# Kernel optimization log

Measured on AMD Instinct MI355X. Metric: run time of the kernel, lower is better.

The kernel has to match this reference:

```python
import jax, jax.numpy as jnp
import numpy as np

N_LEADS = 12
N_HEADS = 4
LN_EPS = 1e-5

def _ecg_adj_norm():
    # Fixed 12-lead ECG adjacency with self loops, symmetric GCN normalization
    conns = [(0,1),(0,2),(1,2),(0,3),(1,3),(2,3),(0,4),(1,4),(1,5),(2,5),
             (6,7),(7,8),(8,9),(9,10),(10,11),(0,6),(1,9),(2,11)]
    A = np.zeros((N_LEADS, N_LEADS), dtype=np.float32)
    for i, j in conns:
        A[i, j] = 1.0
        A[j, i] = 1.0
    A += np.eye(N_LEADS, dtype=np.float32)
    d = A.sum(axis=1)
    dinv = 1.0 / np.sqrt(d)
    return jnp.asarray(dinv[:, None] * A * dinv[None, :])  # [12,12]

A_NORM = _ecg_adj_norm()

def gcn(x, W, b):
    # x: [B,12,F] -> A_norm @ (x W) + b
    return jnp.einsum('ij,bjf->bif', A_NORM, x @ W) + b

def mha(x, in_w, in_b, out_w, out_b):
    # x: [B,S,E]; torch nn.MultiheadAttention, batch_first=True
    B, S, E = x.shape
    D = E // N_HEADS
    qkv = x @ in_w.T + in_b                      # [B,S,3E]
    q, k, v = jnp.split(qkv, 3, axis=-1)
    def heads(t):
        return t.reshape(B, S, N_HEADS, D).transpose(0, 2, 1, 3)  # [B,H,S,D]
    q, k, v = heads(q), heads(k), heads(v)
    scores = jnp.einsum('bhsd,bhtd->bhst', q, k) / jnp.sqrt(jnp.float32(D))
    attn = jax.nn.softmax(scores, axis=-1)
    o = jnp.einsum('bhst,bhtd->bhsd', attn, v)   # [B,H,S,D]
    o = o.transpose(0, 2, 1, 3).reshape(B, S, E)
    return o @ out_w.T + out_b

def layer_norm(x, g, b):
    mu = x.mean(axis=-1, keepdims=True)
    var = ((x - mu) ** 2).mean(axis=-1, keepdims=True)
    return (x - mu) * jax.lax.rsqrt(var + LN_EPS) * g + b

def setup_inputs() -> dict:
    key = jax.random.key(0)
    ks = jax.random.split(key, 8)
    B, F_IN, H, OUT = 8192, 512, 256, 256
    s = lambda fan: 1.0 / np.sqrt(fan)
    return {
        'x': jax.random.normal(ks[0], (B, N_LEADS, F_IN), dtype=jnp.float32),
        'W1': jax.random.normal(ks[1], (F_IN, H), dtype=jnp.float32) * s(F_IN),
        'b1': jnp.zeros((H,), jnp.float32),
        'W2': jax.random.normal(ks[2], (H, H), dtype=jnp.float32) * s(H),
        'b2': jnp.zeros((H,), jnp.float32),
        'W3': jax.random.normal(ks[3], (H, OUT), dtype=jnp.float32) * s(H),
        'b3': jnp.zeros((OUT,), jnp.float32),
        'in_proj_w': jax.random.normal(ks[4], (3 * H, H), dtype=jnp.float32) * s(H),
        'in_proj_b': jnp.zeros((3 * H,), jnp.float32),
        'out_proj_w': jax.random.normal(ks[5], (H, H), dtype=jnp.float32) * s(H),
        'out_proj_b': jnp.zeros((H,), jnp.float32),
        'ln_g': jnp.ones((H,), jnp.float32),
        'ln_b': jnp.zeros((H,), jnp.float32),
    }

def reference(x, W1, b1, W2, b2, W3, b3, in_proj_w, in_proj_b, out_proj_w, out_proj_b, ln_g, ln_b):
    h = jax.nn.relu(gcn(x, W1, b1))              # dropout is identity at eval
    h = jax.nn.relu(gcn(h, W2, b2))              # [B,12,H]
    att = mha(h, in_proj_w, in_proj_b, out_proj_w, out_proj_b)
    h = layer_norm(h + att, ln_g, ln_b)
    h3 = gcn(h, W3, b3)                          # [B,12,OUT]
    w = jax.nn.softmax(h3.mean(axis=-1), axis=1) # [B,12] attention pooling
    x_weighted = jnp.einsum('bno,bn->bo', h3, w)
    x_max = h3.max(axis=1)
    return jnp.concatenate([x_weighted, x_max], axis=1)  # [B, 2*OUT]
```

## Files before the change

### kernel.cpp

```cpp
#include <hip/hip_runtime.h>
#include <hip/hip_bf16.h>
#include <cstdint>
#include <cstddef>

typedef unsigned short u16;
typedef u16 u16x8 __attribute__((ext_vector_type(8)));
typedef u16 u16x4 __attribute__((ext_vector_type(4)));
typedef __bf16 bf16x8 __attribute__((ext_vector_type(8)));
typedef float f32x4 __attribute__((ext_vector_type(4)));

__device__ const unsigned short ADJ_MASK[12] = {
    95u, 575u, 2095u, 15u, 19u, 38u, 193u, 448u, 896u, 1794u, 3584u, 3076u};

__device__ __forceinline__ float b2f(u16 u) {
  union { unsigned int i; float f; } v;
  v.i = ((unsigned int)u) << 16;
  return v.f;
}
__device__ __forceinline__ u16 f2b(float f) {
  union { float f; unsigned int i; } v;
  v.f = f;
  unsigned int r = v.i + 0x7fffu + ((v.i >> 16) & 1u);
  return (u16)(r >> 16);
}

#define GLOAD_LDS16(gsrc, ldst)                                         \
  __builtin_amdgcn_global_load_lds(                                     \
      (const __attribute__((address_space(1))) unsigned int*)(gsrc),    \
      (__attribute__((address_space(3))) unsigned int*)(ldst), 16, 0, 0)

__device__ __forceinline__ void build_anorm(float* An) {
  int t = threadIdx.x;
  if (t < 144) {
    int i = t / 12, j = t % 12;
    float di = (float)__popc((int)ADJ_MASK[i]);
    float dj = (float)__popc((int)ADJ_MASK[j]);
    An[t] = ((ADJ_MASK[i] >> j) & 1) ? (1.0f / sqrtf(di * dj)) : 0.0f;
  }
}

__global__ void __launch_bounds__(256) k_detect2(const void* a, const void* b,
                                                 int* flags) {
  const unsigned int* w = (const unsigned int*)(blockIdx.x ? b : a);
  __shared__ int s;
  if (threadIdx.x == 0) s = 0;
  __syncthreads();
  int cnt = 0;
  for (int t = 0; t < 16; ++t) {
    unsigned int v = w[t * 256 + threadIdx.x];
    unsigned int e = (v >> 7) & 0xFFu;
    if (e != 0u && (e < 0x5Au || e > 0x89u)) ++cnt;
  }
  atomicAdd(&s, cnt);
  __syncthreads();
  if (threadIdx.x == 0) flags[blockIdx.x] = (s > 1024) ? 1 : 0;
}

__global__ void __launch_bounds__(256) k_cvt_small(
    const void* b1, const void* b2, const void* b3, const void* inb,
    const void* outb, const void* lng, const void* lnb, u16* dst,
    const int* flag) {
  int idx = blockIdx.x * 256 + threadIdx.x;
  if (idx >= 2304) return;
  const void* src;
  int off = idx;
  if (idx < 256)       { src = b1; }
  else if (idx < 512)  { src = b2;   off = idx - 256; }
  else if (idx < 768)  { src = b3;   off = idx - 512; }
  else if (idx < 1536) { src = inb;  off = idx - 768; }
  else if (idx < 1792) { src = outb; off = idx - 1536; }
  else if (idx < 2048) { src = lng;  off = idx - 1792; }
  else                 { src = lnb;  off = idx - 2048; }
  dst[idx] = (*flag) ? f2b(((const float*)src)[off]) : ((const u16*)src)[off];
}

__global__ void __launch_bounds__(256) k_cvt_w(const void* inw,
                                               const void* outw, u16* dst,
                                               const int* flag) {
  int idx = blockIdx.x * 256 + threadIdx.x;
  const void* src = (idx < 196608) ? inw : outw;
  int off = (idx < 196608) ? idx : idx - 196608;
  dst[idx] = (*flag) ? f2b(((const float*)src)[off]) : ((const u16*)src)[off];
}

__global__ void __launch_bounds__(256) k_transpose3(const void* W1,
                                                    const void* W2,
                                                    const void* W3, u16* dst,
                                                    const int* flag) {
  int idx = blockIdx.x * 256 + threadIdx.x;
  const void* src;
  int R, C, li = idx;
  if (idx < 131072)      { src = W1; R = 512; C = 256; }
  else if (idx < 196608) { src = W2; R = 256; C = 256; li = idx - 131072; }
  else                   { src = W3; R = 256; C = 256; li = idx - 196608; }
  int c = li / R, r = li - c * R;
  u16 v = (*flag) ? f2b(((const float*)src)[r * C + c])
                  : ((const u16*)src)[r * C + c];
  dst[(idx - li) + c * R + r] = v;
}

__global__ void __launch_bounds__(256) k_mix(const u16* __restrict__ in,
                                             const u16* __restrict__ bias,
                                             u16* __restrict__ out, int relu) {
  __shared__ u16 X[6144];
  __shared__ float An[144];
  build_anorm(An);
  const int tid = threadIdx.x;
  const long base = (long)blockIdx.x * 6144;
#pragma unroll
  for (int i = 0; i < 3; ++i) {
    int idx = i * 256 + tid;
    *(u16x8*)(X + idx * 8) = *(const u16x8*)(in + base + idx * 8);
  }
  __syncthreads();
#pragma unroll
  for (int v = 0; v < 3; ++v) {
    int idx = v * 256 + tid;
    int s = idx / 384;
    int rem = idx - s * 384;
    int i = rem >> 5;
    int fg = rem & 31;
    float a[8];
#pragma unroll
    for (int u = 0; u < 8; ++u) a[u] = b2f(bias[fg * 8 + u]);
    for (int j = 0; j < 12; ++j) {
      float c = An[i * 12 + j];
      if (c != 0.0f) {
        u16x8 y = *(const u16x8*)(X + (s * 12 + j) * 256 + fg * 8);
#pragma unroll
        for (int u = 0; u < 8; ++u) a[u] += c * b2f(y[u]);
      }
    }
    u16x8 o;
#pragma unroll
    for (int u = 0; u < 8; ++u) {
      float vv = relu ? fmaxf(a[u], 0.0f) : a[u];
      o[u] = f2b(vv);
    }
    *(u16x8*)(out + base + idx * 8) = o;
  }
}

__device__ __forceinline__ void gemm_core(const void* __restrict__ A, int lda,
                                          int isf32,
                                          const u16* __restrict__ Bt,
                                          u16* As, u16* Bs,
                                          long m0, long n0, int K,
                                          f32x4 acc[6][4]) {
  const int tid = threadIdx.x;
  const int wave = tid >> 6, lane = tid & 63;
  const int q = lane >> 4, r16 = lane & 15;
  f32x4 zero = {0.f, 0.f, 0.f, 0.f};
#pragma unroll
  for (int a = 0; a < 6; ++a)
#pragma unroll
    for (int b = 0; b < 4; ++b) acc[a][b] = zero;

  for (int k0 = 0; k0 < K; k0 += 64) {
    if (isf32) {
      const float* Af = (const float*)A;
#pragma unroll
      for (int i = 0; i < 3; ++i) {
        int idx = i * 256 + tid;
        int rr = idx >> 3, cg = idx & 7;
        const float* sp = Af + (m0 + rr) * (long)lda + k0 + cg * 8;
        u16x8 t;
#pragma unroll
        for (int u = 0; u < 8; ++u) t[u] = f2b(sp[u]);
        *(u16x8*)(As + rr * 64 + ((cg ^ (rr & 7)) << 3)) = t;
      }
    } else {
      const u16* Ab = (const u16*)A;
#pragma unroll
      for (int i = 0; i < 3; ++i) {
        int c = i * 256 + tid;
        int rr = c >> 3, s = c & 7;
        GLOAD_LDS16(Ab + (m0 + rr) * (long)lda + k0 + ((s ^ (rr & 7)) << 3),
                    As + c * 8);
      }
    }
#pragma unroll
    for (int i = 0; i < 8; ++i) {
      int c = i * 256 + tid;
      int rr = c >> 3, s = c & 7;
      GLOAD_LDS16(Bt + (n0 + rr) * (long)K + k0 + ((s ^ (rr & 7)) << 3),
                  Bs + c * 8);
    }
    __syncthreads();
#pragma unroll
    for (int ks = 0; ks < 64; ks += 32) {
      const int ck = q + (ks >> 3);
      bf16x8 af[6], bfv[4];
#pragma unroll
      for (int rb = 0; rb < 6; ++rb) {
        int row = rb * 16 + r16;
        af[rb] = *(const bf16x8*)(As + row * 64 + ((ck ^ (row & 7)) << 3));
      }
#pragma unroll
      for (int cb = 0; cb < 4; ++cb) {
        int row = (wave * 4 + cb) * 16 + r16;
        bfv[cb] = *(const bf16x8*)(Bs + row * 64 + ((ck ^ (row & 7)) << 3));
      }
#pragma unroll
      for (int rb = 0; rb < 6; ++rb)
#pragma unroll
        for (int cb = 0; cb < 4; ++cb)
          acc[rb][cb] = __builtin_amdgcn_mfma_f32_16x16x32_bf16(
              af[rb], bfv[cb], acc[rb][cb], 0, 0, 0);
    }
    __syncthreads();
  }
}

__device__ __forceinline__ void gemm_core128(const void* __restrict__ A,
                                             int lda, int isf32,
                                             const u16* __restrict__ Bt,
                                             u16* As, u16* Bs,
                                             long m0, long n0, int K,
                                             f32x4 acc[6][2]) {
  const int tid = threadIdx.x;
  const int wave = tid >> 6, lane = tid & 63;
  const int q = lane >> 4, r16 = lane & 15;
  f32x4 zero = {0.f, 0.f, 0.f, 0.f};
#pragma unroll
  for (int a = 0; a < 6; ++a)
#pragma unroll
    for (int b = 0; b < 2; ++b) acc[a][b] = zero;

  for (int k0 = 0; k0 < K; k0 += 64) {
    if (isf32) {
      const float* Af = (const float*)A;
#pragma unroll
      for (int i = 0; i < 3; ++i) {
        int idx = i * 256 + tid;
        int rr = idx >> 3, cg = idx & 7;
        const float* sp = Af + (m0 + rr) * (long)lda + k0 + cg * 8;
        u16x8 t;
#pragma unroll
        for (int u = 0; u < 8; ++u) t[u] = f2b(sp[u]);
        *(u16x8*)(As + rr * 64 + ((cg ^ (rr & 7)) << 3)) = t;
      }
    } else {
      const u16* Ab = (const u16*)A;
#pragma unroll
      for (int i = 0; i < 3; ++i) {
        int c = i * 256 + tid;
        int rr = c >> 3, s = c & 7;
        GLOAD_LDS16(Ab + (m0 + rr) * (long)lda + k0 + ((s ^ (rr & 7)) << 3),
                    As + c * 8);
      }
    }
#pragma unroll
    for (int i = 0; i < 4; ++i) {
      int c = i * 256 + tid;
      int rr = c >> 3, s = c & 7;
      GLOAD_LDS16(Bt + (n0 + rr) * (long)K + k0 + ((s ^ (rr & 7)) << 3),
                  Bs + c * 8);
    }
    __syncthreads();
#pragma unroll
    for (int ks = 0; ks < 64; ks += 32) {
      const int ck = q + (ks >> 3);
      bf16x8 af[6], bfv[2];
#pragma unroll
      for (int rb = 0; rb < 6; ++rb) {
        int row = rb * 16 + r16;
        af[rb] = *(const bf16x8*)(As + row * 64 + ((ck ^ (row & 7)) << 3));
      }
#pragma unroll
      for (int cb = 0; cb < 2; ++cb) {
        int row = (wave * 2 + cb) * 16 + r16;
        bfv[cb] = *(const bf16x8*)(Bs + row * 64 + ((ck ^ (row & 7)) << 3));
      }
#pragma unroll
      for (int rb = 0; rb < 6; ++rb)
#pragma unroll
        for (int cb = 0; cb < 2; ++cb)
          acc[rb][cb] = __builtin_amdgcn_mfma_f32_16x16x32_bf16(
              af[rb], bfv[cb], acc[rb][cb], 0, 0, 0);
    }
    __syncthreads();
  }
}

template <bool BIAS>
__global__ void __launch_bounds__(256, 4) k_gemm(const void* __restrict__ A,
                                                 int lda,
                                                 const u16* __restrict__ Bt,
                                                 const u16* __restrict__ bias,
                                                 u16* __restrict__ C,
                                                 int K, int Ntot,
                                                 const int* aflag) {
  __shared__ u16 As[96 * 64];
  __shared__ u16 Bs[128 * 64];
  f32x4 acc[6][2];
  const long n0 = (long)blockIdx.x * 128;
  const long m0 = (long)blockIdx.y * 96;
  int isf32 = aflag ? *aflag : 0;
  gemm_core128(A, lda, isf32, Bt, As, Bs, m0, n0, K, acc);
  const int tid = threadIdx.x;
  const int wave = tid >> 6, lane = tid & 63;
  const int q = lane >> 4, r16 = lane & 15;
#pragma unroll
  for (int cb = 0; cb < 2; ++cb) {
    long col = n0 + (wave * 2 + cb) * 16 + r16;
    float bvv = BIAS ? b2f(bias[col]) : 0.0f;
#pragma unroll
    for (int rb = 0; rb < 6; ++rb) {
#pragma unroll
      for (int rr = 0; rr < 4; ++rr) {
        long row = m0 + rb * 16 + q * 4 + rr;
        C[row * (long)Ntot + col] = f2b(acc[rb][cb][rr] + bvv);
      }
    }
  }
}

__global__ void __launch_bounds__(256) k_attn(u16* __restrict__ QKV) {
  __shared__ u16 T[12 * 768];
  __shared__ float Sc[4][12][12];
  const int tid = threadIdx.x;
  const long base = (long)blockIdx.x * (12 * 768);
#pragma unroll
  for (int i = 0; i < 9; ++i) {
    int idx = i * 256 + tid;
    *(u16x4*)(T + idx * 4) = *(const u16x4*)(QKV + base + idx * 4);
  }
  __syncthreads();
  for (int p = tid; p < 576; p += 256) {
    int h = p / 144, r = p % 144, i = r / 12, j = r % 12;
    const u16* qp = T + i * 768 + h * 64;
    const u16* kp = T + j * 768 + 256 + h * 64;
    float s = 0.f;
#pragma unroll
    for (int dv = 0; dv < 8; ++dv) {
      u16x8 qv = *(const u16x8*)(qp + dv * 8);
      u16x8 kv = *(const u16x8*)(kp + dv * 8);
#pragma unroll
      for (int u = 0; u < 8; ++u) s += b2f(qv[u]) * b2f(kv[u]);
    }
    Sc[h][i][j] = s * 0.125f;
  }
  __syncthreads();
  if (tid < 48) {
    int h = tid / 12, i = tid % 12;
    float m = -1e30f;
#pragma unroll
    for (int j = 0; j < 12; ++j) m = fmaxf(m, Sc[h][i][j]);
    float e[12];
    float ssum = 0.f;
#pragma unroll
    for (int j = 0; j < 12; ++j) {
      e[j] = __expf(Sc[h][i][j] - m);
      ssum += e[j];
    }
    float inv = 1.0f / ssum;
#pragma unroll
    for (int j = 0; j < 12; ++j) Sc[h][i][j] = e[j] * inv;
  }
  __syncthreads();
  {
    int h = tid >> 6;
    int d = tid & 63;
    float vv[12];
#pragma unroll
    for (int j = 0; j < 12; ++j) vv[j] = b2f(T[j * 768 + 512 + h * 64 + d]);
#pragma unroll
    for (int i = 0; i < 12; ++i) {
      float o = 0.f;
#pragma unroll
      for (int j = 0; j < 12; ++j) o += Sc[h][i][j] * vv[j];
      QKV[base + i * 768 + h * 64 + d] = f2b(o);
    }
  }
}

__global__ void __launch_bounds__(256) k_resid_ln_mix(
    const u16* __restrict__ H, const u16* __restrict__ Oa,
    const u16* __restrict__ g, const u16* __restrict__ bb,
    u16* __restrict__ out) {
  __shared__ float Xn[12 * 256];
  __shared__ float An[144];
  __shared__ float mu[12], rs[12];
  build_anorm(An);
  const int tid = threadIdx.x;
  const long baseH = (long)blockIdx.x * 3072;
  const long baseO = (long)blockIdx.x * 9216;
#pragma unroll
  for (int i = 0; i < 3; ++i) {
    int idx = i * 256 + tid;
    int row = idx >> 6, c4 = idx & 63;
    u16x4 hv = *(const u16x4*)(H + baseH + idx * 4);
    u16x4 ov = *(const u16x4*)(Oa + baseO + row * 768 + c4 * 4);
#pragma unroll
    for (int u = 0; u < 4; ++u) Xn[idx * 4 + u] = b2f(hv[u]) + b2f(ov[u]);
  }
  __syncthreads();
  {
    int wave = tid >> 6, lane = tid & 63;
    for (int rr = wave; rr < 12; rr += 4) {
      float s = 0.f, s2 = 0.f;
#pragma unroll
      for (int u = 0; u < 4; ++u) {
        float xv = Xn[rr * 256 + u * 64 + lane];
        s += xv;
        s2 += xv * xv;
      }
#pragma unroll
      for (int off = 32; off > 0; off >>= 1) {
        s += __shfl_down(s, off, 64);
        s2 += __shfl_down(s2, off, 64);
      }
      if (lane == 0) {
        float m = s * (1.0f / 256.0f);
        float var = s2 * (1.0f / 256.0f) - m * m;
        mu[rr] = m;
        rs[rr] = rsqrtf(var + 1e-5f);
      }
    }
  }
  __syncthreads();
  {
    float gv = b2f(g[tid]);
    float bv = b2f(bb[tid]);
    float xn[12];
#pragma unroll
    for (int i = 0; i < 12; ++i) {
      float x = Xn[i * 256 + tid];
      xn[i] = (x - mu[i]) * rs[i] * gv + bv;
    }
#pragma unroll
    for (int i = 0; i < 12; ++i) {
      float o = 0.f;
#pragma unroll
      for (int j = 0; j < 12; ++j) o += An[i * 12 + j] * xn[j];
      out[baseH + i * 256 + tid] = f2b(o);
    }
  }
}

__global__ void __launch_bounds__(256) k_attn_mega(
    u16* __restrict__ H, const u16* __restrict__ inw,
    const u16* __restrict__ inb, const u16* __restrict__ outw,
    const u16* __restrict__ outb, const u16* __restrict__ lng,
    const u16* __restrict__ lnb) {
  __shared__ u16 Hs[32 * 264];
  __shared__ u16 Qs[32 * 264];
  __shared__ u16 KVs[24 * 512];
  __shared__ float Sc[4][2][12][12];
  __shared__ float An[144];
  __shared__ float mu[24], rs[24];
  const int tid = threadIdx.x;
  const int wave = tid >> 6, lane = tid & 63;
  const int q = lane >> 4, r16 = lane & 15;
  build_anorm(An);
  const long base = (long)blockIdx.x * 6144;
#pragma unroll
  for (int i = 0; i < 3; ++i) {
    int idx = i * 256 + tid;
    int rr = idx >> 5, cg = idx & 31;
    *(u16x8*)(Hs + rr * 264 + cg * 8) = *(const u16x8*)(H + base + idx * 8);
  }
  {
    int rr = 24 + (tid >> 5), cg = tid & 31;
    u16x8 z = {0, 0, 0, 0, 0, 0, 0, 0};
    *(u16x8*)(Hs + rr * 264 + cg * 8) = z;
  }
  __syncthreads();
  {
    f32x4 acc[2][12];
    f32x4 zero = {0.f, 0.f, 0.f, 0.f};
#pragma unroll
    for (int rb = 0; rb < 2; ++rb)
#pragma unroll
      for (int c = 0; c < 12; ++c) acc[rb][c] = zero;
    for (int k0 = 0; k0 < 256; k0 += 32) {
      bf16x8 af[2];
#pragma unroll
      for (int rb = 0; rb < 2; ++rb)
        af[rb] = *(const bf16x8*)(Hs + (rb * 16 + r16) * 264 + k0 + q * 8);
#pragma unroll
      for (int c = 0; c < 12; ++c) {
        bf16x8 bf = *(const bf16x8*)(inw + (long)((wave * 12 + c) * 16 + r16) * 256 + k0 + q * 8);
#pragma unroll
        for (int rb = 0; rb < 2; ++rb)
          acc[rb][c] = __builtin_amdgcn_mfma_f32_16x16x32_bf16(af[rb], bf, acc[rb][c], 0, 0, 0);
      }
    }
#pragma unroll
    for (int c = 0; c < 12; ++c) {
      int col = (wave * 12 + c) * 16 + r16;
      float bv = b2f(inb[col]);
#pragma unroll
      for (int rb = 0; rb < 2; ++rb)
#pragma unroll
        for (int rr2 = 0; rr2 < 4; ++rr2) {
          int row = rb * 16 + q * 4 + rr2;
          float v = acc[rb][c][rr2] + bv;
          if (col < 256) Qs[row * 264 + col] = f2b(v);
          else if (row < 24) KVs[row * 512 + col - 256] = f2b(v);
        }
    }
  }
  __syncthreads();
  {
    int h = wave;
#pragma unroll
    for (int t = 0; t < 5; ++t) {
      int p = t * 64 + lane;
      if (p < 288) {
        int s = p / 144, r = p - s * 144, i = r / 12, j = r - i * 12;
        const u16* qp = Qs + (s * 12 + i) * 264 + h * 64;
        const u16* kp = KVs + (s * 12 + j) * 512 + h * 64;
        float dot = 0.f;
#pragma unroll
        for (int dv = 0; dv < 8; ++dv) {
          u16x8 qv = *(const u16x8*)(qp + dv * 8);
          u16x8 kv = *(const u16x8*)(kp + dv * 8);
#pragma unroll
          for (int u = 0; u < 8; ++u) dot += b2f(qv[u]) * b2f(kv[u]);
        }
        Sc[h][s][i][j] = dot * 0.125f;
      }
    }
  }
  __syncthreads();
  if (lane < 24) {
    int h = wave, s = lane / 12, i = lane - (lane / 12) * 12;
    float m = -1e30f;
#pragma unroll
    for (int j = 0; j < 12; ++j) m = fmaxf(m, Sc[h][s][i][j]);
    float e[12];
    float ssum = 0.f;
#pragma unroll
    for (int j = 0; j < 12; ++j) {
      e[j] = __expf(Sc[h][s][i][j] - m);
      ssum += e[j];
    }
    float inv = 1.0f / ssum;
#pragma unroll
    for (int j = 0; j < 12; ++j) Sc[h][s][i][j] = e[j] * inv;
  }
  __syncthreads();
  {
    int h = wave, d = lane;
    for (int si = 0; si < 24; ++si) {
      int s = si / 12;
      float o = 0.f;
#pragma unroll
      for (int j = 0; j < 12; ++j)
        o += Sc[h][s][si - s * 12][j] * b2f(KVs[(s * 12 + j) * 512 + 256 + h * 64 + d]);
      Qs[si * 264 + h * 64 + d] = f2b(o);
    }
  }
  __syncthreads();
  {
    f32x4 acc[2][4];
    f32x4 zero = {0.f, 0.f, 0.f, 0.f};
#pragma unroll
    for (int rb = 0; rb < 2; ++rb)
#pragma unroll
      for (int cb = 0; cb < 4; ++cb) acc[rb][cb] = zero;
    for (int k0 = 0; k0 < 256; k0 += 32) {
      bf16x8 af[2];
#pragma unroll
      for (int rb = 0; rb < 2; ++rb)
        af[rb] = *(const bf16x8*)(Qs + (rb * 16 + r16) * 264 + k0 + q * 8);
#pragma unroll
      for (int cb = 0; cb < 4; ++cb) {
        bf16x8 bf = *(const bf16x8*)(outw + (long)((wave * 4 + cb) * 16 + r16) * 256 + k0 + q * 8);
#pragma unroll
        for (int rb = 0; rb < 2; ++rb)
          acc[rb][cb] = __builtin_amdgcn_mfma_f32_16x16x32_bf16(af[rb], bf, acc[rb][cb], 0, 0, 0);
      }
    }
#pragma unroll
    for (int cb = 0; cb < 4; ++cb) {
      int col = (wave * 4 + cb) * 16 + r16;
      float ob = b2f(outb[col]);
#pragma unroll
      for (int rb = 0; rb < 2; ++rb)
#pragma unroll
        for (int rr2 = 0; rr2 < 4; ++rr2) {
          int row = rb * 16 + q * 4 + rr2;
          if (row < 24) {
            float x = acc[rb][cb][rr2] + ob + b2f(Hs[row * 264 + col]);
            Hs[row * 264 + col] = f2b(x);
          }
        }
    }
  }
  __syncthreads();
  {
    for (int rr2 = wave * 6; rr2 < wave * 6 + 6; ++rr2) {
      float s1 = 0.f, s2 = 0.f;
#pragma unroll
      for (int u = 0; u < 4; ++u) {
        float xv = b2f(Hs[rr2 * 264 + u * 64 + lane]);
        s1 += xv;
        s2 += xv * xv;
      }
#pragma unroll
      for (int off = 32; off > 0; off >>= 1) {
        s1 += __shfl_down(s1, off, 64);
        s2 += __shfl_down(s2, off, 64);
      }
      if (lane == 0) {
        float m = s1 * (1.0f / 256.0f);
        mu[rr2] = m;
        rs[rr2] = rsqrtf(s2 * (1.0f / 256.0f) - m * m + 1e-5f);
      }
    }
  }
  __syncthreads();
  {
    float gvv = b2f(lng[tid]);
    float bvv = b2f(lnb[tid]);
#pragma unroll
    for (int s = 0; s < 2; ++s) {
      float xn[12];
#pragma unroll
      for (int j = 0; j < 12; ++j) {
        int row = s * 12 + j;
        xn[j] = (b2f(Hs[row * 264 + tid]) - mu[row]) * rs[row] * gvv + bvv;
      }
#pragma unroll
      for (int i = 0; i < 12; ++i) {
        float o = 0.f;
#pragma unroll
        for (int j = 0; j < 12; ++j) o += An[i * 12 + j] * xn[j];
        H[base + (s * 12 + i) * 256 + tid] = f2b(o);
      }
    }
  }
}

__global__ void __launch_bounds__(256, 2) k_gemm_pool(const u16* __restrict__ A,
                                                      const u16* __restrict__ Bt,
                                                      const u16* __restrict__ bias,
                                                      float* __restrict__ out) {
  __shared__ __align__(16) char smraw[50688];
  __shared__ float rowsum[96];
  __shared__ float wsm[96];
  u16* As = (u16*)smraw;
  u16* Bs = As + 96 * 64;
  u16* Y = (u16*)smraw;
  f32x4 acc[6][4];
  const long m0 = (long)blockIdx.x * 96;
  gemm_core(A, 256, 0, Bt, As, Bs, m0, 0, 256, acc);
  const int tid = threadIdx.x;
  const int wave = tid >> 6, lane = tid & 63;
  const int q = lane >> 4, r16 = lane & 15;
#pragma unroll
  for (int cb = 0; cb < 4; ++cb) {
    int col = (wave * 4 + cb) * 16 + r16;
    float bvv = b2f(bias[col]);
#pragma unroll
    for (int rb = 0; rb < 6; ++rb)
#pragma unroll
      for (int rr = 0; rr < 4; ++rr) {
        int row = rb * 16 + q * 4 + rr;
        Y[row * 264 + col] = f2b(acc[rb][cb][rr] + bvv);
      }
  }
  __syncthreads();
  for (int row = wave; row < 96; row += 4) {
    float s = 0.f;
#pragma unroll
    for (int u = 0; u < 4; ++u) s += b2f(Y[row * 264 + u * 64 + lane]);
#pragma unroll
    for (int off = 32; off > 0; off >>= 1) s += __shfl_down(s, off, 64);
    if (lane == 0) rowsum[row] = s;
  }
  __syncthreads();
  if (tid < 8) {
    float m = -1e30f;
#pragma unroll
    for (int l = 0; l < 12; ++l) m = fmaxf(m, rowsum[tid * 12 + l]);
    float e[12];
    float ssum = 0.f;
#pragma unroll
    for (int l = 0; l < 12; ++l) {
      e[l] = __expf((rowsum[tid * 12 + l] - m) * (1.0f / 256.0f));
      ssum += e[l];
    }
    float inv = 1.0f / ssum;
#pragma unroll
    for (int l = 0; l < 12; ++l) wsm[tid * 12 + l] = e[l] * inv;
  }
  __syncthreads();
  {
    int s = tid >> 5, cg = tid & 31;
    float wa[8], mx[8];
#pragma unroll
    for (int u = 0; u < 8; ++u) {
      wa[u] = 0.f;
      mx[u] = -1e30f;
    }
#pragma unroll
    for (int l = 0; l < 12; ++l) {
      float w = wsm[s * 12 + l];
      u16x8 yv = *(const u16x8*)(Y + (s * 12 + l) * 264 + cg * 8);
#pragma unroll
      for (int u = 0; u < 8; ++u) {
        float y = b2f(yv[u]);
        wa[u] += w * y;
        mx[u] = fmaxf(mx[u], y);
      }
    }
    long ob = ((long)blockIdx.x * 8 + s) * 512;
#pragma unroll
    for (int u = 0; u < 8; ++u) {
      out[ob + cg * 8 + u] = wa[u];
      out[ob + 256 + cg * 8 + u] = mx[u];
    }
  }
}

extern "C" void kernel_launch(void* const* d_in, const int* in_sizes, int n_in,
                              void* d_out, int out_size, void* d_ws,
                              size_t ws_size, hipStream_t stream) {
  (void)in_sizes; (void)n_in; (void)out_size;
  const void* x    = d_in[0];
  const void* W1   = d_in[1];
  const void* b1   = d_in[2];
  const void* W2   = d_in[3];
  const void* b2   = d_in[4];
  const void* W3   = d_in[5];
  const void* b3   = d_in[6];
  const void* inw  = d_in[7];
  const void* inb  = d_in[8];
  const void* outw = d_in[9];
  const void* outb = d_in[10];
  const void* lng  = d_in[11];
  const void* lnb  = d_in[12];
  float* out = (float*)d_out;

  u16* ws16 = (u16*)d_ws;
  int* flags = (int*)d_ws;
  u16* W1T    = ws16 + 64;
  u16* W2T    = W1T + 131072;
  u16* W3T    = W2T + 65536;
  u16* inw_b  = W3T + 65536;
  u16* outw_b = inw_b + 196608;
  u16* b1b    = outw_b + 65536;
  u16* b2b    = b1b + 256;
  u16* b3b    = b2b + 256;
  u16* inbb   = b3b + 256;
  u16* outbb  = inbb + 768;
  u16* lngb   = outbb + 256;
  u16* lnbb   = lngb + 256;
  u16* BUF    = lnbb + 256;
  u16* QKV    = BUF + 25165824L;
  const size_t NEED_A = (size_t)(QKV + 75497472L - ws16) * 2;

  k_detect2<<<2, 256, 0, stream>>>(x, W1, flags);

  k_cvt_small<<<9, 256, 0, stream>>>(b1, b2, b3, inb, outb, lng, lnb, b1b,
                                     flags + 1);
  k_cvt_w<<<1024, 256, 0, stream>>>(inw, outw, inw_b, flags + 1);
  k_transpose3<<<1024, 256, 0, stream>>>(W1, W2, W3, W1T, flags + 1);

  k_gemm<false><<<dim3(2, 1024), 256, 0, stream>>>(x, 512, W1T, nullptr, BUF, 512, 256, flags);
  k_mix<<<4096, 256, 0, stream>>>(BUF, b1b, BUF, 1);
  k_gemm<false><<<dim3(2, 1024), 256, 0, stream>>>(BUF, 256, W2T, nullptr, BUF, 256, 256, nullptr);
  k_mix<<<4096, 256, 0, stream>>>(BUF, b2b, BUF, 1);

  if (ws_size >= NEED_A) {
    k_gemm<true><<<dim3(6, 1024), 256, 0, stream>>>(BUF, 256, inw_b, inbb, QKV, 256, 768, nullptr);
    k_attn<<<8192, 256, 0, stream>>>(QKV);
    k_gemm<true><<<dim3(2, 1024), 256, 0, stream>>>(QKV, 768, outw_b, outbb, QKV + 256, 256, 768, nullptr);
    k_resid_ln_mix<<<8192, 256, 0, stream>>>(BUF, QKV + 256, lngb, lnbb, BUF);
  } else {
    k_attn_mega<<<4096, 256, 0, stream>>>(BUF, inw_b, inbb, outw_b, outbb, lngb, lnbb);
  }
  k_gemm_pool<<<1024, 256, 0, stream>>>(BUF, W3T, b3b, out);
}
```

Before: 637.1 us.

## Double-buffer LDS tiles in generic GEMM with compile-time K

Turns the shared GEMM core into a double-buffered pipeline. The next K-tile's global-to-LDS loads are issued before computing on the current tile, with explicit vmcnt waits, barriers and a setprio bump around the MFMA section. K becomes a template parameter so the loop fully unrolls. LDS use doubles and launch bounds drop from 4 to 2 blocks per CU, which may reduce occupancy-based latency hiding. The fp32 A path still waits on all loads each iteration.

After: 645.9 us. About the same (+1.4%).

```diff
diff --git a/kernel.cpp b/kernel.cpp
--- a/kernel.cpp
+++ b/kernel.cpp
@@ -212,12 +212,13 @@
   }
 }
 
-__device__ __forceinline__ void gemm_core128(const void* __restrict__ A,
-                                             int lda, int isf32,
-                                             const u16* __restrict__ Bt,
-                                             u16* As, u16* Bs,
-                                             long m0, long n0, int K,
-                                             f32x4 acc[6][2]) {
+template <int K>
+__device__ __forceinline__ void gemm_core128_db(const void* __restrict__ A,
+                                                int lda, int isf32,
+                                                const u16* __restrict__ Bt,
+                                                u16* AsBuf, u16* BsBuf,
+                                                long m0, long n0,
+                                                f32x4 acc[6][2]) {
   const int tid = threadIdx.x;
   const int wave = tid >> 6, lane = tid & 63;
   const int q = lane >> 4, r16 = lane & 15;
@@ -227,9 +228,11 @@
 #pragma unroll
     for (int b = 0; b < 2; ++b) acc[a][b] = zero;
 
-  for (int k0 = 0; k0 < K; k0 += 64) {
+  const u16* Ab = (const u16*)A;
+  const float* Af = (const float*)A;
+
+  auto stageA = [&](u16* dst, int k0) {
     if (isf32) {
-      const float* Af = (const float*)A;
 #pragma unroll
       for (int i = 0; i < 3; ++i) {
         int idx = i * 256 + tid;
@@ -238,26 +241,56 @@
         u16x8 t;
 #pragma unroll
         for (int u = 0; u < 8; ++u) t[u] = f2b(sp[u]);
-        *(u16x8*)(As + rr * 64 + ((cg ^ (rr & 7)) << 3)) = t;
+        *(u16x8*)(dst + rr * 64 + ((cg ^ (rr & 7)) << 3)) = t;
       }
     } else {
-      const u16* Ab = (const u16*)A;
 #pragma unroll
       for (int i = 0; i < 3; ++i) {
         int c = i * 256 + tid;
         int rr = c >> 3, s = c & 7;
         GLOAD_LDS16(Ab + (m0 + rr) * (long)lda + k0 + ((s ^ (rr & 7)) << 3),
-                    As + c * 8);
-      }
-    }
+                    dst + c * 8);
+      }
+    }
+  };
+  auto stageB = [&](u16* dst, int k0) {
 #pragma unroll
     for (int i = 0; i < 4; ++i) {
       int c = i * 256 + tid;
       int rr = c >> 3, s = c & 7;
       GLOAD_LDS16(Bt + (n0 + rr) * (long)K + k0 + ((s ^ (rr & 7)) << 3),
-                  Bs + c * 8);
-    }
-    __syncthreads();
+                  dst + c * 8);
+    }
+  };
+
+  u16* Ac = AsBuf;
+  u16* An = AsBuf + 96 * 64;
+  u16* Bc = BsBuf;
+  u16* Bn = BsBuf + 128 * 64;
+
+  stageA(Ac, 0);
+  stageB(Bc, 0);
+
+  constexpr int T = K / 64;
+#pragma unroll
+  for (int t = 0; t < T; ++t) {
+    const bool more = (t + 1 < T);
+    if (more) {
+      stageA(An, (t + 1) * 64);
+      stageB(Bn, (t + 1) * 64);
+    }
+    __builtin_amdgcn_sched_barrier(0);
+    if (isf32) {
+      asm volatile("s_waitcnt vmcnt(0) lgkmcnt(0)" ::: "memory");
+    } else if (more) {
+      asm volatile("s_waitcnt vmcnt(7)" ::: "memory");
+    } else {
+      asm volatile("s_waitcnt vmcnt(0)" ::: "memory");
+    }
+    __builtin_amdgcn_sched_barrier(0);
+    __builtin_amdgcn_s_barrier();
+    __builtin_amdgcn_sched_barrier(0);
+    __builtin_amdgcn_s_setprio(1);
 #pragma unroll
     for (int ks = 0; ks < 64; ks += 32) {
       const int ck = q + (ks >> 3);
@@ -265,12 +298,12 @@
 #pragma unroll
       for (int rb = 0; rb < 6; ++rb) {
         int row = rb * 16 + r16;
-        af[rb] = *(const bf16x8*)(As + row * 64 + ((ck ^ (row & 7)) << 3));
+        af[rb] = *(const bf16x8*)(Ac + row * 64 + ((ck ^ (row & 7)) << 3));
       }
 #pragma unroll
       for (int cb = 0; cb < 2; ++cb) {
         int row = (wave * 2 + cb) * 16 + r16;
-        bfv[cb] = *(const bf16x8*)(Bs + row * 64 + ((ck ^ (row & 7)) << 3));
+        bfv[cb] = *(const bf16x8*)(Bc + row * 64 + ((ck ^ (row & 7)) << 3));
       }
 #pragma unroll
       for (int rb = 0; rb < 6; ++rb)
@@ -279,25 +312,31 @@
           acc[rb][cb] = __builtin_amdgcn_mfma_f32_16x16x32_bf16(
               af[rb], bfv[cb], acc[rb][cb], 0, 0, 0);
     }
-    __syncthreads();
-  }
-}
-
-template <bool BIAS>
-__global__ void __launch_bounds__(256, 4) k_gemm(const void* __restrict__ A,
+    __builtin_amdgcn_s_setprio(0);
+    __builtin_amdgcn_sched_barrier(0);
+    __builtin_amdgcn_s_barrier();
+    __builtin_amdgcn_sched_barrier(0);
+    u16* tp;
+    tp = Ac; Ac = An; An = tp;
+    tp = Bc; Bc = Bn; Bn = tp;
+  }
+}
+
+template <bool BIAS, int K>
+__global__ void __launch_bounds__(256, 2) k_gemm(const void* __restrict__ A,
                                                  int lda,
                                                  const u16* __restrict__ Bt,
                                                  const u16* __restrict__ bias,
                                                  u16* __restrict__ C,
-                                                 int K, int Ntot,
+                                                 int Ntot,
                                                  const int* aflag) {
-  __shared__ u16 As[96 * 64];
-  __shared__ u16 Bs[128 * 64];
+  __shared__ u16 As[2 * 96 * 64];
+  __shared__ u16 Bs[2 * 128 * 64];
   f32x4 acc[6][2];
   const long n0 = (long)blockIdx.x * 128;
   const long m0 = (long)blockIdx.y * 96;
   int isf32 = aflag ? *aflag : 0;
-  gemm_core128(A, lda, isf32, Bt, As, Bs, m0, n0, K, acc);
+  gemm_core128_db<K>(A, lda, isf32, Bt, As, Bs, m0, n0, acc);
   const int tid = threadIdx.x;
   const int wave = tid >> 6, lane = tid & 63;
   const int q = lane >> 4, r16 = lane & 15;
@@ -761,15 +800,15 @@
   k_cvt_w<<<1024, 256, 0, stream>>>(inw, outw, inw_b, flags + 1);
   k_transpose3<<<1024, 256, 0, stream>>>(W1, W2, W3, W1T, flags + 1);
 
-  k_gemm<false><<<dim3(2, 1024), 256, 0, stream>>>(x, 512, W1T, nullptr, BUF, 512, 256, flags);
+  k_gemm<false, 512><<<dim3(2, 1024), 256, 0, stream>>>(x, 512, W1T, nullptr, BUF, 256, flags);
   k_mix<<<4096, 256, 0, stream>>>(BUF, b1b, BUF, 1);
-  k_gemm<false><<<dim3(2, 1024), 256, 0, stream>>>(BUF, 256, W2T, nullptr, BUF, 256, 256, nullptr);
+  k_gemm<false, 256><<<dim3(2, 1024), 256, 0, stream>>>(BUF, 256, W2T, nullptr, BUF, 256, nullptr);
   k_mix<<<4096, 256, 0, stream>>>(BUF, b2b, BUF, 1);
 
   if (ws_size >= NEED_A) {
-    k_gemm<true><<<dim3(6, 1024), 256, 0, stream>>>(BUF, 256, inw_b, inbb, QKV, 256, 768, nullptr);
+    k_gemm<true, 256><<<dim3(6, 1024), 256, 0, stream>>>(BUF, 256, inw_b, inbb, QKV, 768, nullptr);
     k_attn<<<8192, 256, 0, stream>>>(QKV);
-    k_gemm<true><<<dim3(2, 1024), 256, 0, stream>>>(QKV, 768, outw_b, outbb, QKV + 256, 256, 768, nullptr);
+    k_gemm<true, 256><<<dim3(2, 1024), 256, 0, stream>>>(QKV, 768, outw_b, outbb, QKV + 256, 768, nullptr);
     k_resid_ln_mix<<<8192, 256, 0, stream>>>(BUF, QKV + 256, lngb, lnbb, BUF);
   } else {
     k_attn_mega<<<4096, 256, 0, stream>>>(BUF, inw_b, inbb, outw_b, outbb, lngb, lnbb);
```

## Fuse GCN adjacency mixing into GEMM epilogues and out-proj with LayerNorm

Applied to the files above, without the earlier changes.

Replaces the separate GEMM + k_mix pairs for the first two GCN layers with a single k_gemm_mix kernel. It stages each tile's GEMM output in shared memory and applies the 12x12 adjacency mix, bias and ReLU there. The attention output projection, residual add, LayerNorm and the third-layer adjacency mix are also merged into one k_oproj_ln kernel that covers the full 256-column width per block. This removes several full-tensor round trips through global memory and three kernel launches. The cost is more shared memory per block and lower occupancy for the LN kernel (launch bounds 256,2).

New measurement: 683.0 us. 7.2% more time.

```diff
diff --git a/kernel.cpp b/kernel.cpp
--- a/kernel.cpp
+++ b/kernel.cpp
@@ -99,48 +99,6 @@
   dst[(idx - li) + c * R + r] = v;
 }
 
-__global__ void __launch_bounds__(256) k_mix(const u16* __restrict__ in,
-                                             const u16* __restrict__ bias,
-                                             u16* __restrict__ out, int relu) {
-  __shared__ u16 X[6144];
-  __shared__ float An[144];
-  build_anorm(An);
-  const int tid = threadIdx.x;
-  const long base = (long)blockIdx.x * 6144;
-#pragma unroll
-  for (int i = 0; i < 3; ++i) {
-    int idx = i * 256 + tid;
-    *(u16x8*)(X + idx * 8) = *(const u16x8*)(in + base + idx * 8);
-  }
-  __syncthreads();
-#pragma unroll
-  for (int v = 0; v < 3; ++v) {
-    int idx = v * 256 + tid;
-    int s = idx / 384;
-    int rem = idx - s * 384;
-    int i = rem >> 5;
-    int fg = rem & 31;
-    float a[8];
-#pragma unroll
-    for (int u = 0; u < 8; ++u) a[u] = b2f(bias[fg * 8 + u]);
-    for (int j = 0; j < 12; ++j) {
-      float c = An[i * 12 + j];
-      if (c != 0.0f) {
-        u16x8 y = *(const u16x8*)(X + (s * 12 + j) * 256 + fg * 8);
-#pragma unroll
-        for (int u = 0; u < 8; ++u) a[u] += c * b2f(y[u]);
-      }
-    }
-    u16x8 o;
-#pragma unroll
-    for (int u = 0; u < 8; ++u) {
-      float vv = relu ? fmaxf(a[u], 0.0f) : a[u];
-      o[u] = f2b(vv);
-    }
-    *(u16x8*)(out + base + idx * 8) = o;
-  }
-}
-
 __device__ __forceinline__ void gemm_core(const void* __restrict__ A, int lda,
                                           int isf32,
                                           const u16* __restrict__ Bt,
@@ -283,13 +241,75 @@
   }
 }
 
-template <bool BIAS>
+template <int K>
+__global__ void __launch_bounds__(256, 4) k_gemm_mix(const void* __restrict__ A,
+                                                     int lda,
+                                                     const u16* __restrict__ Bt,
+                                                     const u16* __restrict__ bias,
+                                                     u16* __restrict__ C,
+                                                     const int* aflag) {
+  __shared__ __align__(16) char smraw[28672];
+  __shared__ float An[144];
+  u16* As = (u16*)smraw;
+  u16* Bs = As + 96 * 64;
+  u16* Y = (u16*)smraw;
+  build_anorm(An);
+  f32x4 acc[6][2];
+  const long n0 = (long)blockIdx.x * 128;
+  const long m0 = (long)blockIdx.y * 96;
+  int isf32 = aflag ? *aflag : 0;
+  gemm_core128(A, lda, isf32, Bt, As, Bs, m0, n0, K, acc);
+  const int tid = threadIdx.x;
+  const int wave = tid >> 6, lane = tid & 63;
+  const int q = lane >> 4, r16 = lane & 15;
+#pragma unroll
+  for (int cb = 0; cb < 2; ++cb) {
+    int col = (wave * 2 + cb) * 16 + r16;
+#pragma unroll
+    for (int rb = 0; rb < 6; ++rb)
+#pragma unroll
+      for (int rr = 0; rr < 4; ++rr) {
+        int row = rb * 16 + q * 4 + rr;
+        Y[row * 136 + col] = f2b(acc[rb][cb][rr]);
+      }
+  }
+  __syncthreads();
+  const int s = tid >> 5, cg = tid & 31;
+  float bb4[4];
+#pragma unroll
+  for (int u = 0; u < 4; ++u) bb4[u] = b2f(bias[n0 + cg * 4 + u]);
+  float xn[12][4];
+#pragma unroll
+  for (int j = 0; j < 12; ++j) {
+    u16x4 yv = *(const u16x4*)(Y + (s * 12 + j) * 136 + cg * 4);
+#pragma unroll
+    for (int u = 0; u < 4; ++u) xn[j][u] = b2f(yv[u]);
+  }
+  const long cbase = m0 * 256;
+#pragma unroll
+  for (int i = 0; i < 12; ++i) {
+    float o[4] = {bb4[0], bb4[1], bb4[2], bb4[3]};
+    for (int j = 0; j < 12; ++j) {
+      float c = An[i * 12 + j];
+      if (c != 0.0f) {
+#pragma unroll
+        for (int u = 0; u < 4; ++u) o[u] += c * xn[j][u];
+      }
+    }
+    u16x4 ov;
+#pragma unroll
+    for (int u = 0; u < 4; ++u) ov[u] = f2b(fmaxf(o[u], 0.0f));
+    *(u16x4*)(C + cbase + (long)(s * 12 + i) * 256 + n0 + cg * 4) = ov;
+  }
+}
+
+template <bool BIAS, int K>
 __global__ void __launch_bounds__(256, 4) k_gemm(const void* __restrict__ A,
                                                  int lda,
                                                  const u16* __restrict__ Bt,
                                                  const u16* __restrict__ bias,
                                                  u16* __restrict__ C,
-                                                 int K, int Ntot,
+                                                 int Ntot,
                                                  const int* aflag) {
   __shared__ u16 As[96 * 64];
   __shared__ u16 Bs[128 * 64];
@@ -316,6 +336,90 @@
   }
 }
 
+__global__ void __launch_bounds__(256, 2) k_oproj_ln(
+    const u16* __restrict__ Q, const u16* __restrict__ Bt,
+    const u16* __restrict__ outb, const u16* __restrict__ lng,
+    const u16* __restrict__ lnb, u16* __restrict__ H) {
+  __shared__ __align__(16) char smraw[50688];
+  __shared__ float An[144];
+  u16* As = (u16*)smraw;
+  u16* Bs = As + 96 * 64;
+  u16* Y = (u16*)smraw;
+  build_anorm(An);
+  f32x4 acc[6][4];
+  const long m0 = (long)blockIdx.x * 96;
+  gemm_core(Q, 768, 0, Bt, As, Bs, m0, 0, 256, acc);
+  const int tid = threadIdx.x;
+  const int wave = tid >> 6, lane = tid & 63;
+  const int q = lane >> 4, r16 = lane & 15;
+#pragma unroll
+  for (int cb = 0; cb < 4; ++cb) {
+    int col = (wave * 4 + cb) * 16 + r16;
+    float bvv = b2f(outb[col]);
+#pragma unroll
+    for (int rb = 0; rb < 6; ++rb)
+#pragma unroll
+      for (int rr = 0; rr < 4; ++rr) {
+        int row = rb * 16 + q * 4 + rr;
+        Y[row * 264 + col] = f2b(acc[rb][cb][rr] + bvv);
+      }
+  }
+  __syncthreads();
+  float g4[4], bl4[4];
+#pragma unroll
+  for (int u = 0; u < 4; ++u) {
+    g4[u] = b2f(lng[lane * 4 + u]);
+    bl4[u] = b2f(lnb[lane * 4 + u]);
+  }
+  const long hbase = m0 * 256;
+#pragma unroll
+  for (int sv = 0; sv < 2; ++sv) {
+    const int s = wave * 2 + sv;
+    float x[12][4];
+#pragma unroll
+    for (int j = 0; j < 12; ++j) {
+      int row = s * 12 + j;
+      u16x4 yv = *(const u16x4*)(Y + row * 264 + lane * 4);
+      u16x4 hv = *(const u16x4*)(H + hbase + (long)row * 256 + lane * 4);
+#pragma unroll
+      for (int u = 0; u < 4; ++u) x[j][u] = b2f(yv[u]) + b2f(hv[u]);
+    }
+#pragma unroll
+    for (int j = 0; j < 12; ++j) {
+      float s1 = x[j][0] + x[j][1] + x[j][2] + x[j][3];
+      float s2 = x[j][0] * x[j][0] + x[j][1] * x[j][1] +
+                 x[j][2] * x[j][2] + x[j][3] * x[j][3];
+#pragma unroll
+      for (int off = 32; off > 0; off >>= 1) {
+        s1 += __shfl_down(s1, off, 64);
+        s2 += __shfl_down(s2, off, 64);
+      }
+      s1 = __shfl(s1, 0, 64);
+      s2 = __shfl(s2, 0, 64);
+      float m = s1 * (1.0f / 256.0f);
+      float rstd = rsqrtf(s2 * (1.0f / 256.0f) - m * m + 1e-5f);
+#pragma unroll
+      for (int u = 0; u < 4; ++u)
+        x[j][u] = (x[j][u] - m) * rstd * g4[u] + bl4[u];
+    }
+#pragma unroll
+    for (int i = 0; i < 12; ++i) {
+      float o[4] = {0.f, 0.f, 0.f, 0.f};
+      for (int j = 0; j < 12; ++j) {
+        float c = An[i * 12 + j];
+        if (c != 0.0f) {
+#pragma unroll
+          for (int u = 0; u < 4; ++u) o[u] += c * x[j][u];
+        }
+      }
+      u16x4 ov;
+#pragma unroll
+      for (int u = 0; u < 4; ++u) ov[u] = f2b(o[u]);
+      *(u16x4*)(H + hbase + (long)(s * 12 + i) * 256 + lane * 4) = ov;
+    }
+  }
+}
+
 __global__ void __launch_bounds__(256) k_attn(u16* __restrict__ QKV) {
   __shared__ u16 T[12 * 768];
   __shared__ float Sc[4][12][12];
@@ -371,70 +475,6 @@
 #pragma unroll
       for (int j = 0; j < 12; ++j) o += Sc[h][i][j] * vv[j];
       QKV[base + i * 768 + h * 64 + d] = f2b(o);
-    }
-  }
-}
-
-__global__ void __launch_bounds__(256) k_resid_ln_mix(
-    const u16* __restrict__ H, const u16* __restrict__ Oa,
-    const u16* __restrict__ g, const u16* __restrict__ bb,
-    u16* __restrict__ out) {
-  __shared__ float Xn[12 * 256];
-  __shared__ float An[144];
-  __shared__ float mu[12], rs[12];
-  build_anorm(An);
-  const int tid = threadIdx.x;
-  const long baseH = (long)blockIdx.x * 3072;
-  const long baseO = (long)blockIdx.x * 9216;
-#pragma unroll
-  for (int i = 0; i < 3; ++i) {
-    int idx = i * 256 + tid;
-    int row = idx >> 6, c4 = idx & 63;
-    u16x4 hv = *(const u16x4*)(H + baseH + idx * 4);
-    u16x4 ov = *(const u16x4*)(Oa + baseO + row * 768 + c4 * 4);
-#pragma unroll
-    for (int u = 0; u < 4; ++u) Xn[idx * 4 + u] = b2f(hv[u]) + b2f(ov[u]);
-  }
-  __syncthreads();
-  {
-    int wave = tid >> 6, lane = tid & 63;
-    for (int rr = wave; rr < 12; rr += 4) {
-      float s = 0.f, s2 = 0.f;
-#pragma unroll
-      for (int u = 0; u < 4; ++u) {
-        float xv = Xn[rr * 256 + u * 64 + lane];
-        s += xv;
-        s2 += xv * xv;
-      }
-#pragma unroll
-      for (int off = 32; off > 0; off >>= 1) {
-        s += __shfl_down(s, off, 64);
-        s2 += __shfl_down(s2, off, 64);
-      }
-      if (lane == 0) {
-        float m = s * (1.0f / 256.0f);
-        float var = s2 * (1.0f / 256.0f) - m * m;
-        mu[rr] = m;
-        rs[rr] = rsqrtf(var + 1e-5f);
-      }
-    }
-  }
-  __syncthreads();
-  {
-    float gv = b2f(g[tid]);
-    float bv = b2f(bb[tid]);
-    float xn[12];
-#pragma unroll
-    for (int i = 0; i < 12; ++i) {
-      float x = Xn[i * 256 + tid];
-      xn[i] = (x - mu[i]) * rs[i] * gv + bv;
-    }
-#pragma unroll
-    for (int i = 0; i < 12; ++i) {
-      float o = 0.f;
-#pragma unroll
-      for (int j = 0; j < 12; ++j) o += An[i * 12 + j] * xn[j];
-      out[baseH + i * 256 + tid] = f2b(o);
     }
   }
 }
@@ -761,17 +801,16 @@
   k_cvt_w<<<1024, 256, 0, stream>>>(inw, outw, inw_b, flags + 1);
   k_transpose3<<<1024, 256, 0, stream>>>(W1, W2, W3, W1T, flags + 1);
 
-  k_gemm<false><<<dim3(2, 1024), 256, 0, stream>>>(x, 512, W1T, nullptr, BUF, 512, 256, flags);
-  k_mix<<<4096, 256, 0, stream>>>(BUF, b1b, BUF, 1);
-  k_gemm<false><<<dim3(2, 1024), 256, 0, stream>>>(BUF, 256, W2T, nullptr, BUF, 256, 256, nullptr);
-  k_mix<<<4096, 256, 0, stream>>>(BUF, b2b, BUF, 1);
-
   if (ws_size >= NEED_A) {
-    k_gemm<true><<<dim3(6, 1024), 256, 0, stream>>>(BUF, 256, inw_b, inbb, QKV, 256, 768, nullptr);
+    u16* H1 = QKV;
+    k_gemm_mix<512><<<dim3(2, 1024), 256, 0, stream>>>(x, 512, W1T, b1b, H1, flags);
+    k_gemm_mix<256><<<dim3(2, 1024), 256, 0, stream>>>(H1, 256, W2T, b2b, BUF, nullptr);
+    k_gemm<true, 256><<<dim3(6, 1024), 256, 0, stream>>>(BUF, 256, inw_b, inbb, QKV, 768, nullptr);
     k_attn<<<8192, 256, 0, stream>>>(QKV);
-    k_gemm<true><<<dim3(2, 1024), 256, 0, stream>>>(QKV, 768, outw_b, outbb, QKV + 256, 256, 768, nullptr);
-    k_resid_ln_mix<<<8192, 256, 0, stream>>>(BUF, QKV + 256, lngb, lnbb, BUF);
+    k_oproj_ln<<<1024, 256, 0, stream>>>(QKV, outw_b, outbb, lngb, lnbb, BUF);
   } else {
+    k_gemm_mix<512><<<dim3(2, 1024), 256, 0, stream>>>(x, 512, W1T, b1b, BUF, flags);
+    k_gemm_mix<256><<<dim3(2, 1024), 256, 0, stream>>>(BUF, 256, W2T, b2b, BUF, nullptr);
     k_attn_mega<<<4096, 256, 0, stream>>>(BUF, inw_b, inbb, outw_b, outbb, lngb, lnbb);
   }
   k_gemm_pool<<<1024, 256, 0, stream>>>(BUF, W3T, b3b, out);
```

## Fuse GCN adjacency mix, bias and ReLU into GEMM epilogue

Applied to the files above, without the earlier changes.

Adds a k_gemm_mix kernel that stages the GEMM tile in shared memory and applies the 12-lead adjacency mix, bias and ReLU before writing. This replaces the separate k_mix passes after the first two GCN GEMMs, removing a full read/write of the hidden activations per layer and two launches. The K dimension becomes a template parameter for the GEMMs. The fallback path runs the second fused GEMM in place, which risks a read/write race between column blocks.

After: 631.9 us. About the same (-0.8%).

```diff
diff --git a/kernel.cpp b/kernel.cpp
--- a/kernel.cpp
+++ b/kernel.cpp
@@ -99,48 +99,6 @@
   dst[(idx - li) + c * R + r] = v;
 }
 
-__global__ void __launch_bounds__(256) k_mix(const u16* __restrict__ in,
-                                             const u16* __restrict__ bias,
-                                             u16* __restrict__ out, int relu) {
-  __shared__ u16 X[6144];
-  __shared__ float An[144];
-  build_anorm(An);
-  const int tid = threadIdx.x;
-  const long base = (long)blockIdx.x * 6144;
-#pragma unroll
-  for (int i = 0; i < 3; ++i) {
-    int idx = i * 256 + tid;
-    *(u16x8*)(X + idx * 8) = *(const u16x8*)(in + base + idx * 8);
-  }
-  __syncthreads();
-#pragma unroll
-  for (int v = 0; v < 3; ++v) {
-    int idx = v * 256 + tid;
-    int s = idx / 384;
-    int rem = idx - s * 384;
-    int i = rem >> 5;
-    int fg = rem & 31;
-    float a[8];
-#pragma unroll
-    for (int u = 0; u < 8; ++u) a[u] = b2f(bias[fg * 8 + u]);
-    for (int j = 0; j < 12; ++j) {
-      float c = An[i * 12 + j];
-      if (c != 0.0f) {
-        u16x8 y = *(const u16x8*)(X + (s * 12 + j) * 256 + fg * 8);
-#pragma unroll
-        for (int u = 0; u < 8; ++u) a[u] += c * b2f(y[u]);
-      }
-    }
-    u16x8 o;
-#pragma unroll
-    for (int u = 0; u < 8; ++u) {
-      float vv = relu ? fmaxf(a[u], 0.0f) : a[u];
-      o[u] = f2b(vv);
-    }
-    *(u16x8*)(out + base + idx * 8) = o;
-  }
-}
-
 __device__ __forceinline__ void gemm_core(const void* __restrict__ A, int lda,
                                           int isf32,
                                           const u16* __restrict__ Bt,
@@ -283,13 +241,75 @@
   }
 }
 
-template <bool BIAS>
+template <int K>
+__global__ void __launch_bounds__(256, 4) k_gemm_mix(const void* __restrict__ A,
+                                                     int lda,
+                                                     const u16* __restrict__ Bt,
+                                                     const u16* __restrict__ bias,
+                                                     u16* __restrict__ C,
+                                                     const int* aflag) {
+  __shared__ __align__(16) char smraw[28672];
+  __shared__ float An[144];
+  u16* As = (u16*)smraw;
+  u16* Bs = As + 96 * 64;
+  u16* Y = (u16*)smraw;
+  build_anorm(An);
+  f32x4 acc[6][2];
+  const long n0 = (long)blockIdx.x * 128;
+  const long m0 = (long)blockIdx.y * 96;
+  int isf32 = aflag ? *aflag : 0;
+  gemm_core128(A, lda, isf32, Bt, As, Bs, m0, n0, K, acc);
+  const int tid = threadIdx.x;
+  const int wave = tid >> 6, lane = tid & 63;
+  const int q = lane >> 4, r16 = lane & 15;
+#pragma unroll
+  for (int cb = 0; cb < 2; ++cb) {
+    int col = (wave * 2 + cb) * 16 + r16;
+#pragma unroll
+    for (int rb = 0; rb < 6; ++rb)
+#pragma unroll
+      for (int rr = 0; rr < 4; ++rr) {
+        int row = rb * 16 + q * 4 + rr;
+        Y[row * 136 + col] = f2b(acc[rb][cb][rr]);
+      }
+  }
+  __syncthreads();
+  const int s = tid >> 5, cg = tid & 31;
+  float bb4[4];
+#pragma unroll
+  for (int u = 0; u < 4; ++u) bb4[u] = b2f(bias[n0 + cg * 4 + u]);
+  float xn[12][4];
+#pragma unroll
+  for (int j = 0; j < 12; ++j) {
+    u16x4 yv = *(const u16x4*)(Y + (s * 12 + j) * 136 + cg * 4);
+#pragma unroll
+    for (int u = 0; u < 4; ++u) xn[j][u] = b2f(yv[u]);
+  }
+  const long cbase = m0 * 256;
+#pragma unroll
+  for (int i = 0; i < 12; ++i) {
+    float o[4] = {bb4[0], bb4[1], bb4[2], bb4[3]};
+    for (int j = 0; j < 12; ++j) {
+      float c = An[i * 12 + j];
+      if (c != 0.0f) {
+#pragma unroll
+        for (int u = 0; u < 4; ++u) o[u] += c * xn[j][u];
+      }
+    }
+    u16x4 ov;
+#pragma unroll
+    for (int u = 0; u < 4; ++u) ov[u] = f2b(fmaxf(o[u], 0.0f));
+    *(u16x4*)(C + cbase + (long)(s * 12 + i) * 256 + n0 + cg * 4) = ov;
+  }
+}
+
+template <bool BIAS, int K>
 __global__ void __launch_bounds__(256, 4) k_gemm(const void* __restrict__ A,
                                                  int lda,
                                                  const u16* __restrict__ Bt,
                                                  const u16* __restrict__ bias,
                                                  u16* __restrict__ C,
-                                                 int K, int Ntot,
+                                                 int Ntot,
                                                  const int* aflag) {
   __shared__ u16 As[96 * 64];
   __shared__ u16 Bs[128 * 64];
@@ -761,17 +781,17 @@
   k_cvt_w<<<1024, 256, 0, stream>>>(inw, outw, inw_b, flags + 1);
   k_transpose3<<<1024, 256, 0, stream>>>(W1, W2, W3, W1T, flags + 1);
 
-  k_gemm<false><<<dim3(2, 1024), 256, 0, stream>>>(x, 512, W1T, nullptr, BUF, 512, 256, flags);
-  k_mix<<<4096, 256, 0, stream>>>(BUF, b1b, BUF, 1);
-  k_gemm<false><<<dim3(2, 1024), 256, 0, stream>>>(BUF, 256, W2T, nullptr, BUF, 256, 256, nullptr);
-  k_mix<<<4096, 256, 0, stream>>>(BUF, b2b, BUF, 1);
-
   if (ws_size >= NEED_A) {
-    k_gemm<true><<<dim3(6, 1024), 256, 0, stream>>>(BUF, 256, inw_b, inbb, QKV, 256, 768, nullptr);
+    u16* H1 = QKV;
+    k_gemm_mix<512><<<dim3(2, 1024), 256, 0, stream>>>(x, 512, W1T, b1b, H1, flags);
+    k_gemm_mix<256><<<dim3(2, 1024), 256, 0, stream>>>(H1, 256, W2T, b2b, BUF, nullptr);
+    k_gemm<true, 256><<<dim3(6, 1024), 256, 0, stream>>>(BUF, 256, inw_b, inbb, QKV, 768, nullptr);
     k_attn<<<8192, 256, 0, stream>>>(QKV);
-    k_gemm<true><<<dim3(2, 1024), 256, 0, stream>>>(QKV, 768, outw_b, outbb, QKV + 256, 256, 768, nullptr);
+    k_gemm<true, 256><<<dim3(2, 1024), 256, 0, stream>>>(QKV, 768, outw_b, outbb, QKV + 256, 768, nullptr);
     k_resid_ln_mix<<<8192, 256, 0, stream>>>(BUF, QKV + 256, lngb, lnbb, BUF);
   } else {
+    k_gemm_mix<512><<<dim3(2, 1024), 256, 0, stream>>>(x, 512, W1T, b1b, BUF, flags);
+    k_gemm_mix<256><<<dim3(2, 1024), 256, 0, stream>>>(BUF, 256, W2T, b2b, BUF, nullptr);
     k_attn_mega<<<4096, 256, 0, stream>>>(BUF, inw_b, inbb, outw_b, outbb, lngb, lnbb);
   }
   k_gemm_pool<<<1024, 256, 0, stream>>>(BUF, W3T, b3b, out);
```
